# Optimization experiments

Hardware: AMD Instinct MI355X
Metric: run time of the kernel (lower is better)

## Reference

```python
import jax, jax.numpy as jnp
import numpy as np

BATCH = 16384
NUM_NEURONS = 4096
BLOCK_SIZE = 128
NUM_BLOCKS = NUM_NEURONS // BLOCK_SIZE


def setup_inputs() -> dict:
    key = jax.random.key(0)
    k_v, k_dx, k_a, k_b = jax.random.split(key, 4)
    v = jax.random.normal(k_v, (BATCH, NUM_NEURONS), dtype=jnp.float32)
    dx = jax.random.normal(k_dx, (BATCH, 2), dtype=jnp.float32)
    # torch init: rand * 0.002 - 0.001  (uniform in [-0.001, 0.001])
    A_modules = jax.random.uniform(k_a, (NUM_BLOCKS, BLOCK_SIZE, BLOCK_SIZE), dtype=jnp.float32) * 0.002 - 0.001
    B_modules = jax.random.uniform(k_b, (NUM_NEURONS, 2), dtype=jnp.float32) * 0.002 - 0.001
    b = jnp.zeros((), dtype=jnp.float32)
    return {"v": v, "dx": dx, "A_modules": A_modules, "B_modules": B_modules, "b": b}


def reference(v, dx, A_modules, B_modules, b):
    # v @ block_diag(A_modules) == per-block matmul on reshaped v.
    bsz, n = v.shape                      # [B, N]
    nb, bs, _ = A_modules.shape           # [nb, bs, bs], N = nb*bs
    vb = v.reshape(bsz, nb, bs)           # [B, nb, bs]
    vA = jnp.einsum('bnk,nkj->bnj', vb, A_modules).reshape(bsz, n)  # [B, N]
    # dx @ B^T + scalar bias, fused with ReLU
    return jax.nn.relu(vA + dx @ B_modules.T + b)
```

## Files before the change

kernel.cpp:

```cpp
#include <hip/hip_runtime.h>

typedef __attribute__((ext_vector_type(8))) short  bf16x8;
typedef __attribute__((ext_vector_type(4))) float  f32x4;

static __device__ __forceinline__ unsigned short f2bf(float f) {
    unsigned u = __float_as_uint(f);
    u += 0x7fffu + ((u >> 16) & 1u);
    return (unsigned short)(u >> 16);
}

__global__ __launch_bounds__(256) void prep_at_kernel(
        const float* __restrict__ A, unsigned short* __restrict__ At)
{
    int g   = blockIdx.x * 256 + threadIdx.x;
    int bn  = g >> 11;
    int rem = g & 2047;
    int kc  = rem >> 7;
    int n   = rem & 127;

    const float* src = A + bn * 16384 + kc * 8 * 128 + n;
    unsigned h[4];
    #pragma unroll
    for (int j = 0; j < 4; ++j) {
        unsigned short lo = f2bf(src[(2 * j    ) * 128]);
        unsigned short hi = f2bf(src[(2 * j + 1) * 128]);
        h[j] = (unsigned)lo | ((unsigned)hi << 16);
    }
    uint4 pk = make_uint4(h[0], h[1], h[2], h[3]);
    *(uint4*)(At + bn * 16384 + n * 128 + kc * 8) = pk;
}

__global__ __launch_bounds__(512, 4) void trans_main_kernel(
        const float* __restrict__ v,  const float* __restrict__ dx,
        const unsigned short* __restrict__ At, const float* __restrict__ Bm,
        const float* __restrict__ bsc, float* __restrict__ out)
{
    __shared__ float  lds[3][32 * 128];
    __shared__ float2 dxl[1024];

    const int tid = threadIdx.x;
    const int wid = tid >> 6;
    const int l   = tid & 63;
    const int lr  = l & 15;
    const int lq  = l >> 4;
    const int wm  = wid >> 2;
    const int wn  = wid & 3;
    const int bn     = blockIdx.x >> 4;
    const int mtbase = blockIdx.x & 15;

    bf16x8 bq[4][2];
    const unsigned short* atb = At + bn * 16384 + (wn * 32 + lr) * 128 + lq * 8;
    #pragma unroll
    for (int kq = 0; kq < 4; ++kq)
        #pragma unroll
        for (int ni = 0; ni < 2; ++ni)
            bq[kq][ni] = *(const bf16x8*)(atb + ni * 16 * 128 + kq * 32);

    const float bias = *bsc;
    const int col0 = bn * 128 + wn * 32;
    float2 bc[2];
    #pragma unroll
    for (int ni = 0; ni < 2; ++ni)
        bc[ni] = *(const float2*)(Bm + 2 * (col0 + ni * 16 + lr));

    #pragma unroll
    for (int it = 0; it < 2; ++it) {
        int idx  = it * 512 + tid;
        int kk   = idx >> 5;
        int r    = idx & 31;
        int grow = (kk * 16 + mtbase) * 32 + r;
        dxl[idx] = *(const float2*)(dx + 2 * grow);
    }

    auto stage = [&](int buf, int k) {
        const float* src = v + (size_t)(k * 16 + mtbase) * 32 * 4096 + bn * 128;
        #pragma unroll
        for (int it = 0; it < 2; ++it) {
            int c16  = it * 512 + tid;
            int row  = c16 >> 5;
            int off  = (c16 & 31) << 4;
            int soff = off ^ ((row & 7) << 4);
            const float* g = src + (size_t)row * 4096 + (soff >> 2);
            __builtin_amdgcn_global_load_lds(
                (const __attribute__((address_space(1))) unsigned int*)g,
                (__attribute__((address_space(3))) unsigned int*)
                    &lds[buf][c16 * 4],
                16, 0, 0);
        }
    };

    auto body = [&](int buf, int k) {
        const int mt = k * 16 + mtbase;
        f32x4 acc[2];
        acc[0] = (f32x4){0.f, 0.f, 0.f, 0.f};
        acc[1] = (f32x4){0.f, 0.f, 0.f, 0.f};

        const char* Lb = (const char*)&lds[buf][0];
        const int row = wm * 16 + lr;
        const int rb  = row * 512;
        const int m   = (row & 7) << 4;
        #pragma unroll
        for (int kq = 0; kq < 4; ++kq) {
            const int base = kq * 128 + lq * 32;
            float4 f0 = *(const float4*)(Lb + rb + ((base     ) ^ m));
            float4 f1 = *(const float4*)(Lb + rb + ((base + 16) ^ m));
            union { bf16x8 vv; unsigned short s[8]; } u;
            u.s[0] = f2bf(f0.x); u.s[1] = f2bf(f0.y);
            u.s[2] = f2bf(f0.z); u.s[3] = f2bf(f0.w);
            u.s[4] = f2bf(f1.x); u.s[5] = f2bf(f1.y);
            u.s[6] = f2bf(f1.z); u.s[7] = f2bf(f1.w);
            acc[0] = __builtin_amdgcn_mfma_f32_16x16x32_bf16(
                         u.vv, bq[kq][0], acc[0], 0, 0, 0);
            acc[1] = __builtin_amdgcn_mfma_f32_16x16x32_bf16(
                         u.vv, bq[kq][1], acc[1], 0, 0, 0);
        }

        #pragma unroll
        for (int jj = 0; jj < 4; ++jj) {
            const int rl   = k * 32 + wm * 16 + lq * 4 + jj;
            const int rowg = mt * 32 + wm * 16 + lq * 4 + jj;
            const float2 d = dxl[rl];
            float* orow = out + (size_t)rowg * 4096 + col0 + lr;
            float v0 = acc[0][jj] + d.x * bc[0].x + d.y * bc[0].y + bias;
            float v1 = acc[1][jj] + d.x * bc[1].x + d.y * bc[1].y + bias;
            orow[0]  = fmaxf(v0, 0.0f);
            orow[16] = fmaxf(v1, 0.0f);
        }
    };

    __syncthreads();

    stage(0, 0);
    stage(1, 1);

    asm volatile("s_waitcnt vmcnt(2) lgkmcnt(0)" ::: "memory");
    __builtin_amdgcn_s_barrier();
    __builtin_amdgcn_sched_barrier(0);
    stage(2, 2);
    body(0, 0);

    asm volatile("s_waitcnt vmcnt(10) lgkmcnt(0)" ::: "memory");
    __builtin_amdgcn_s_barrier();
    __builtin_amdgcn_sched_barrier(0);
    stage(0, 3);
    body(1, 1);

    for (int k = 2; k < 31; ++k) {
        asm volatile("s_waitcnt vmcnt(18) lgkmcnt(0)" ::: "memory");
        __builtin_amdgcn_s_barrier();
        __builtin_amdgcn_sched_barrier(0);
        if (k + 2 < 32) stage((k + 2) % 3, k + 2);
        body(k % 3, k);
    }

    asm volatile("s_waitcnt vmcnt(16) lgkmcnt(0)" ::: "memory");
    __builtin_amdgcn_s_barrier();
    __builtin_amdgcn_sched_barrier(0);
    body(31 % 3, 31);
}

extern "C" void kernel_launch(void* const* d_in, const int* in_sizes, int n_in,
                              void* d_out, int out_size, void* d_ws, size_t ws_size,
                              hipStream_t stream)
{
    const float* v  = (const float*)d_in[0];
    const float* dx = (const float*)d_in[1];
    const float* A  = (const float*)d_in[2];
    const float* Bm = (const float*)d_in[3];
    const float* b  = (const float*)d_in[4];

    unsigned short* At = (unsigned short*)d_ws;

    prep_at_kernel<<<dim3(256), dim3(256), 0, stream>>>(A, At);
    trans_main_kernel<<<dim3(512), dim3(512), 0, stream>>>(v, dx, At, Bm, b,
                                                           (float*)d_out);
}
```

Baseline: 107.0 us.

## Halve block size and give each block a contiguous row range

The main kernel now launches 1024 blocks of 256 threads, each processing 16-row tiles instead of 32. Each block walks 512 contiguous rows rather than rows strided across the batch. The dx values are loaded asynchronously into LDS with global_load_lds instead of through registers. The aim is smaller per-block LDS, more resident blocks and better DRAM locality for the memory-bound stream. The cost is twice as many blocks, and each block's A fragments are reused over half as many rows.

```diff
diff --git a/kernel.cpp b/kernel.cpp
--- a/kernel.cpp
+++ b/kernel.cpp
@@ -30,23 +30,21 @@
     *(uint4*)(At + bn * 16384 + n * 128 + kc * 8) = pk;
 }
 
-__global__ __launch_bounds__(512, 4) void trans_main_kernel(
+__global__ __launch_bounds__(256) void trans_main_kernel(
         const float* __restrict__ v,  const float* __restrict__ dx,
         const unsigned short* __restrict__ At, const float* __restrict__ Bm,
         const float* __restrict__ bsc, float* __restrict__ out)
 {
-    __shared__ float  lds[3][32 * 128];
-    __shared__ float2 dxl[1024];
+    __shared__ float  lds[3][16 * 128];
+    __shared__ float2 dxl[512];
 
     const int tid = threadIdx.x;
-    const int wid = tid >> 6;
+    const int wn  = tid >> 6;
     const int l   = tid & 63;
     const int lr  = l & 15;
     const int lq  = l >> 4;
-    const int wm  = wid >> 2;
-    const int wn  = wid & 3;
-    const int bn     = blockIdx.x >> 4;
-    const int mtbase = blockIdx.x & 15;
+    const int bn  = blockIdx.x >> 5;
+    const int g   = blockIdx.x & 31;
 
     bf16x8 bq[4][2];
     const unsigned short* atb = At + bn * 16384 + (wn * 32 + lr) * 128 + lq * 8;
@@ -63,26 +61,24 @@
     for (int ni = 0; ni < 2; ++ni)
         bc[ni] = *(const float2*)(Bm + 2 * (col0 + ni * 16 + lr));
 
-    #pragma unroll
-    for (int it = 0; it < 2; ++it) {
-        int idx  = it * 512 + tid;
-        int kk   = idx >> 5;
-        int r    = idx & 31;
-        int grow = (kk * 16 + mtbase) * 32 + r;
-        dxl[idx] = *(const float2*)(dx + 2 * grow);
-    }
+    __builtin_amdgcn_global_load_lds(
+        (const __attribute__((address_space(1))) unsigned int*)
+            (dx + (size_t)g * 1024 + tid * 4),
+        (__attribute__((address_space(3))) unsigned int*)
+            ((char*)dxl + tid * 16),
+        16, 0, 0);
 
     auto stage = [&](int buf, int k) {
-        const float* src = v + (size_t)(k * 16 + mtbase) * 32 * 4096 + bn * 128;
+        const float* src = v + (size_t)(g * 32 + k) * 16 * 4096 + bn * 128;
         #pragma unroll
         for (int it = 0; it < 2; ++it) {
-            int c16  = it * 512 + tid;
+            int c16  = it * 256 + tid;
             int row  = c16 >> 5;
             int off  = (c16 & 31) << 4;
             int soff = off ^ ((row & 7) << 4);
-            const float* g = src + (size_t)row * 4096 + (soff >> 2);
+            const float* gp = src + (size_t)row * 4096 + (soff >> 2);
             __builtin_amdgcn_global_load_lds(
-                (const __attribute__((address_space(1))) unsigned int*)g,
+                (const __attribute__((address_space(1))) unsigned int*)gp,
                 (__attribute__((address_space(3))) unsigned int*)
                     &lds[buf][c16 * 4],
                 16, 0, 0);
@@ -90,15 +86,13 @@
     };
 
     auto body = [&](int buf, int k) {
-        const int mt = k * 16 + mtbase;
         f32x4 acc[2];
         acc[0] = (f32x4){0.f, 0.f, 0.f, 0.f};
         acc[1] = (f32x4){0.f, 0.f, 0.f, 0.f};
 
         const char* Lb = (const char*)&lds[buf][0];
-        const int row = wm * 16 + lr;
-        const int rb  = row * 512;
-        const int m   = (row & 7) << 4;
+        const int rb = lr * 512;
+        const int m  = (lr & 7) << 4;
         #pragma unroll
         for (int kq = 0; kq < 4; ++kq) {
             const int base = kq * 128 + lq * 32;
@@ -117,10 +111,9 @@
 
         #pragma unroll
         for (int jj = 0; jj < 4; ++jj) {
-            const int rl   = k * 32 + wm * 16 + lq * 4 + jj;
-            const int rowg = mt * 32 + wm * 16 + lq * 4 + jj;
-            const float2 d = dxl[rl];
-            float* orow = out + (size_t)rowg * 4096 + col0 + lr;
+            const int rloc = k * 16 + lq * 4 + jj;
+            const float2 d = dxl[rloc];
+            float* orow = out + (size_t)(g * 512 + rloc) * 4096 + col0 + lr;
             float v0 = acc[0][jj] + d.x * bc[0].x + d.y * bc[0].y + bias;
             float v1 = acc[1][jj] + d.x * bc[1].x + d.y * bc[1].y + bias;
             orow[0]  = fmaxf(v0, 0.0f);
@@ -172,6 +165,6 @@
     unsigned short* At = (unsigned short*)d_ws;
 
     prep_at_kernel<<<dim3(256), dim3(256), 0, stream>>>(A, At);
-    trans_main_kernel<<<dim3(512), dim3(512), 0, stream>>>(v, dx, At, Bm, b,
-                                                           (float*)d_out);
+    trans_main_kernel<<<dim3(1024), dim3(256), 0, stream>>>(v, dx, At, Bm, b,
+                                                            (float*)d_out);
 }
```

Measured after the change: 140.2 us. 31.0% more time.
